# Kernel optimization log

Measured on AMD Instinct MI355X. Metric: run time of the kernel, lower is better.

Reference implementation:

```python
import jax, jax.numpy as jnp
import numpy as np

# --- physics constants (match init_kwargs) ---
LX = LY = 0.2
NX = NY = 256
DT = 2.5e-5
N_STEPS = 300
RHO = 1000.0
CS = 5.0
MU = RHO * CS * CS
ETA = 0.1
BULK_DAMPING = 0.01
SOURCE_SIGMA = 0.003
N_PML = 20
MAX_DAMPING = 0.05
PHYSICS_EPS = 1e-8
DX = LX / NX
DY = LY / NY
INV_DX = 1.0 / DX
INV_DY = 1.0 / DY
DT_OVER_RHO = DT / RHO


def _build_damping():
    # cosine-tapered PML profile, exactly as the torch loop
    i = jnp.arange(N_PML, dtype=jnp.float32)
    arg = jnp.pi * (N_PML - i) / N_PML
    factor = 1.0 - MAX_DAMPING * (0.5 + 0.5 * jnp.cos(arg))
    dx_prof = jnp.ones(NX, dtype=jnp.float32)
    dx_prof = dx_prof.at[:N_PML].set(factor)
    dx_prof = dx_prof.at[NX - N_PML:].set(factor[::-1])
    dy_prof = jnp.ones(NY, dtype=jnp.float32)
    dy_prof = dy_prof.at[:N_PML].set(factor)
    dy_prof = dy_prof.at[NY - N_PML:].set(factor[::-1])
    return jnp.outer(dx_prof, dy_prof)  # [nx, ny]


def _grids():
    x = jnp.linspace(DX / 2, LX - DX / 2, NX, dtype=jnp.float32)
    y = jnp.linspace(DY / 2, LY - DY / 2, NY, dtype=jnp.float32)
    return x[:, None], y[None, :]  # broadcastable grid_x, grid_y


def setup_inputs() -> dict:
    key = jax.random.key(0)
    # source trajectory in meters, kept inside the interior (away from PML)
    trajectory = 0.05 + 0.1 * jax.random.uniform(key, (N_STEPS, 2), dtype=jnp.float32)
    return {"trajectory": trajectory}


def reference(trajectory):
    damping = _build_damping()
    gx, gy = _grids()
    amp = 1.0

    def step(carry, xy):
        vz, strain_xz, strain_yz = carry  # each [nx, ny]
        x_t, y_t = xy[0], xy[1]
        # Gaussian source centered at (x_t, y_t)
        r_sq = (gx - x_t) ** 2 + (gy - y_t) ** 2
        source = amp * jnp.exp(-r_sq / (2.0 * SOURCE_SIGMA ** 2))
        # forward differences of vz (zero at trailing edge)
        dvz_dx = jnp.pad((vz[1:, :] - vz[:-1, :]) * INV_DX, ((0, 1), (0, 0)))
        dvz_dy = jnp.pad((vz[:, 1:] - vz[:, :-1]) * INV_DY, ((0, 0), (0, 1)))
        # Kelvin-Voigt stress
        strain_xz = strain_xz + dvz_dx * DT
        strain_yz = strain_yz + dvz_dy * DT
        sigma_xz = MU * strain_xz + ETA * dvz_dx
        sigma_yz = MU * strain_yz + ETA * dvz_dy
        # backward differences of stress (zero at leading edge)
        ds_dx = jnp.pad((sigma_xz[1:, :] - sigma_xz[:-1, :]) * INV_DX, ((1, 0), (0, 0)))
        ds_dy = jnp.pad((sigma_yz[:, 1:] - sigma_yz[:, :-1]) * INV_DY, ((0, 0), (1, 0)))
        # velocity update + bulk damping + PML damping
        vz = vz + DT_OVER_RHO * (ds_dx + ds_dy + source)
        vz = vz * (1.0 - BULK_DAMPING * DT)
        vz = vz * damping
        stress_mag = jnp.sqrt(sigma_xz ** 2 + sigma_yz ** 2 + PHYSICS_EPS)
        return (vz, strain_xz, strain_yz), (vz, stress_mag)

    z = jnp.zeros((NX, NY), dtype=jnp.float32)
    _, (vz_history, stress_history) = jax.lax.scan(step, (z, z, z), trajectory)
    return vz_history, stress_history
```

## Files before the change

kernel.cpp:

```cpp
#include <hip/hip_runtime.h>
#include <math.h>

typedef float v2f __attribute__((ext_vector_type(2)));

#define NX 256
#define NY 256
#define N_STEPS 300
#define N_CELLS (NX * NY)
#define TILE 16
#define HALO 8
#define LSTR 36
#define LROWS 34
#define LIDX(rr, cc) (((rr) + 1) * LSTR + ((cc) + 2))
#define NBX 16
#define NBY 16
#define NCHUNK 38

#define kINV_DX       1280.0f
#define kINV_DY       1280.0f
#define kDT           2.5e-5f
#define kMU           25000.0f
#define kETA          0.1f
#define kDT_OVER_RHO  2.5e-8f
#define kONE_MINUS_BD 0.99999975f
#define kNEG_INV_2SIG2 (-55555.5546875f)
#define kDX           7.8125e-4f
#define kEPS          1e-8f
#define kSRC_SKIP_D2  9.0e-4f

__device__ __forceinline__ float dprof(int k) {
    int m = min(k, NX - 1 - k);
    if (m >= 20) return 1.0f;
    float arg = 3.14159265358979f * (float)(20 - m) / 20.0f;
    return 1.0f - 0.05f * (0.5f + 0.5f * cosf(arg));
}

__device__ __forceinline__ void st_f2(float* p, v2f v) {
    union { v2f f; unsigned long long u; } x;
    x.f = v;
    __hip_atomic_store((unsigned long long*)p, x.u,
                       __ATOMIC_RELAXED, __HIP_MEMORY_SCOPE_AGENT);
}
__device__ __forceinline__ v2f ld_f2(const float* p) {
    union { unsigned long long u; v2f f; } x;
    x.u = __hip_atomic_load((const unsigned long long*)p,
                            __ATOMIC_RELAXED, __HIP_MEMORY_SCOPE_AGENT);
    return x.f;
}
__device__ __forceinline__ float ld_f1(const float* p) {
    union { unsigned u; float f; } x;
    x.u = __hip_atomic_load((const unsigned*)p,
                            __ATOMIC_RELAXED, __HIP_MEMORY_SCOPE_AGENT);
    return x.f;
}

__global__ __launch_bounds__(512, 1) void persist_kernel(
    const float2* __restrict__ traj,
    float* __restrict__ out,
    float* __restrict__ ws,
    unsigned* __restrict__ seq)
{
    __shared__ float s_vz[2][LROWS * LSTR];

    float* vzS[2]  = { ws + 0 * N_CELLS, ws + 1 * N_CELLS };
    float* sxzS[2] = { ws + 2 * N_CELLS, ws + 3 * N_CELLS };
    float* syzS[2] = { ws + 4 * N_CELLS, ws + 5 * N_CELLS };

    const int tid = threadIdx.x;
    const int bid = blockIdx.x;
    const int bx  = bid & (NBX - 1), by = bid >> 4;
    const int r   = tid >> 4;
    const int c0  = (tid & 15) << 1;

    const int gi  = by * TILE + r  - HALO;
    const int gj0 = bx * TILE + c0 - HALO;
    const int g   = gi * NY + gj0;

    const bool rowOK  = (gi >= 0) && (gi < NX);
    const bool colOK  = (gj0 >= 0) && (gj0 < NY);
    const bool inD    = rowOK && colOK;
    const bool haloUp   = (gi - 1 >= 0) && (gi - 1 < NX) && colOK;
    const bool haloLeft = rowOK && (gj0 - 1 >= 0);

    const float mxF  = (gi < NX - 1)      ? kINV_DX : 0.0f;
    const float myF1 = (gj0 + 1 < NY - 1) ? kINV_DY : 0.0f;
    const float mbX  = (gi > 0)           ? kINV_DX : 0.0f;
    const float mbY0 = (gj0 > 0)          ? kINV_DY : 0.0f;
    const v2f mx2  = {mxF, mxF};
    const v2f my2  = {kINV_DY, myF1};
    const v2f mbx2 = {mbX, mbX};
    const v2f mby2 = {mbY0, kINV_DY};

    const float dpx = rowOK ? dprof(gi) : 0.0f;
    const v2f damp2 = { inD ? dpx * dprof(gj0) * kONE_MINUS_BD : 0.0f,
                        inD ? dpx * dprof(gj0 + 1) * kONE_MINUS_BD : 0.0f };
    const float xi  = ((float)gi + 0.5f) * kDX;
    const v2f   yy2 = { ((float)gj0 + 0.5f) * kDX, ((float)gj0 + 1.5f) * kDX };

    const bool owned = (r >= HALO) && (r < HALO + TILE) &&
                       (c0 >= HALO) && (c0 + 1 < HALO + TILE);

    const float xlo = ((float)(by * TILE - HALO) + 0.5f) * kDX;
    const float xhi = ((float)(by * TILE + TILE + HALO - 1) + 0.5f) * kDX;
    const float ylo = ((float)(bx * TILE - HALO) + 0.5f) * kDX;
    const float yhi = ((float)(bx * TILE + TILE + HALO - 1) + 0.5f) * kDX;

    bool isPoller = false; int pollIdx = 0;
    if (tid < 8) {
        const int q  = tid + (tid >= 4);
        const int dy = q / 3 - 1, dx = q % 3 - 1;
        const int nbx_ = bx + dx, nby_ = by + dy;
        if (nbx_ >= 0 && nbx_ < NBX && nby_ >= 0 && nby_ < NBY) {
            isPoller = true;
            pollIdx = (nby_ * NBX + nbx_) * 4;
        }
    }

    for (int idx = tid; idx < 2 * LROWS * LSTR; idx += 512)
        ((float*)s_vz)[idx] = 0.0f;

    v2f V = {0.f, 0.f}, SX = {0.f, 0.f}, SY = {0.f, 0.f}, SXM = {0.f, 0.f};
    float symv = 0.f;
    __syncthreads();

    for (int ch = 0; ch < NCHUNK; ++ch) {
        if (ch > 0) {
            if (isPoller) {
                const unsigned tgt = (unsigned)ch;
                while (__hip_atomic_load(&seq[pollIdx], __ATOMIC_RELAXED,
                                         __HIP_MEMORY_SCOPE_AGENT) < tgt) {
                    __builtin_amdgcn_s_sleep(1);
                }
            }
            __syncthreads();

            if (!owned) {
                const int rs = (ch - 1) & 1;
                v2f nV = {0.f, 0.f}, nSX = {0.f, 0.f}, nSY = {0.f, 0.f};
                v2f nSXM = {0.f, 0.f};
                float nsym = 0.f;
                if (inD) {
                    nV  = ld_f2(&vzS[rs][g]);
                    nSX = ld_f2(&sxzS[rs][g]);
                    nSY = ld_f2(&syzS[rs][g]);
                }
                if (haloUp)   nSXM = ld_f2(&sxzS[rs][g - NY]);
                if (haloLeft) nsym = ld_f1(&syzS[rs][g - 1]);
                V = nV; SX = nSX; SY = nSY; SXM = nSXM; symv = nsym;
            }
        }

        *(v2f*)&s_vz[0][LIDX(r, c0)] = V;
        __syncthreads();

        const int t0 = ch * 8;
        float trx[8], tryy[8];
        #pragma unroll
        for (int s = 0; s < 8; ++s) {
            const int t = t0 + s;
            float2 t2 = (t < N_STEPS) ? traj[t] : make_float2(0.f, 0.f);
            trx[s] = t2.x; tryy[s] = t2.y;
        }

        bool srcNear = false;
        #pragma unroll
        for (int s = 0; s < 8; ++s) {
            const float ddx = fmaxf(fmaxf(xlo - trx[s], trx[s] - xhi), 0.0f);
            const float ddy = fmaxf(fmaxf(ylo - tryy[s], tryy[s] - yhi), 0.0f);
            if (ddx * ddx + ddy * ddy < kSRC_SKIP_D2) srcNear = true;
        }

        v2f hv[8], hs[8];
        #pragma unroll
        for (int s = 0; s < 8; ++s) {
            const int cur = s & 1, nxt = cur ^ 1;

            const v2f vp = *(const v2f*)&s_vz[cur][LIDX(r + 1, c0)];
            const v2f vm = *(const v2f*)&s_vz[cur][LIDX(r - 1, c0)];
            const float vr2 = s_vz[cur][LIDX(r, c0 + 2)];
            const float vl1 = s_vz[cur][LIDX(r, c0 - 1)];

            const v2f dvx = (vp - V) * mx2;
            const v2f vsh = {V.y, vr2};
            const v2f dvy = (vsh - V) * my2;

            SX += dvx * kDT;
            SY += dvy * kDT;
            const v2f GX = SX * kMU + dvx * kETA;
            const v2f GY = SY * kMU + dvy * kETA;

            const v2f dxm = (V - vm) * kINV_DX;
            SXM += dxm * kDT;
            const v2f GXM = SXM * kMU + dxm * kETA;
            const float dym = (V.x - vl1) * kINV_DY;
            symv += dym * kDT;
            const float gym = kMU * symv + kETA * dym;

            const v2f gsh = {gym, GX.x * 0.0f + GY.x};
            v2f ds = (GX - GXM) * mbx2 + (GY - gsh) * mby2;

            if (srcNear) {
                const float rx  = xi - trx[s];
                const float rx2 = rx * rx;
                const v2f ry  = yy2 - tryy[s];
                const v2f arg = (ry * ry + rx2) * kNEG_INV_2SIG2;
                ds += (v2f){__expf(arg.x), __expf(arg.y)};
            }

            V = (V + ds * kDT_OVER_RHO) * damp2;

            if (s < 7) *(v2f*)&s_vz[nxt][LIDX(r, c0)] = V;

            hv[s] = V;
            const v2f g2 = GX * GX + GY * GY + kEPS;
            hs[s] = (v2f){__builtin_amdgcn_sqrtf(g2.x),
                          __builtin_amdgcn_sqrtf(g2.y)};

            if (s < 7) __syncthreads();
        }

        if (owned && ch < NCHUNK - 1) {
            const int wsI = ch & 1;
            st_f2(&vzS[wsI][g],  V);
            st_f2(&sxzS[wsI][g], SX);
            st_f2(&syzS[wsI][g], SY);
        }
        __syncthreads();
        if (ch < NCHUNK - 1 && tid == 0) {
            __hip_atomic_store(&seq[bid * 4], (unsigned)(ch + 1),
                               __ATOMIC_RELAXED, __HIP_MEMORY_SCOPE_AGENT);
        }

        if (owned) {
            #pragma unroll
            for (int s = 0; s < 8; ++s) {
                if (t0 + s < N_STEPS) {
                    *(v2f*)&out[(size_t)(t0 + s) * N_CELLS + g] = hv[s];
                    *(v2f*)&out[(size_t)(N_STEPS + t0 + s) * N_CELLS + g] = hs[s];
                }
            }
        }
    }
}

extern "C" void kernel_launch(void* const* d_in, const int* in_sizes, int n_in,
                              void* d_out, int out_size, void* d_ws, size_t ws_size,
                              hipStream_t stream) {
    const float2* traj = (const float2*)d_in[0];
    float* out = (float*)d_out;
    float* ws  = (float*)d_ws;
    unsigned* seq = (unsigned*)((char*)d_ws + (size_t)6 * N_CELLS * sizeof(float));

    hipMemsetAsync(seq, 0, NBX * NBY * 4 * sizeof(unsigned), stream);

    void* args[] = { (void*)&traj, (void*)&out, (void*)&ws, (void*)&seq };
    hipLaunchCooperativeKernel((const void*)persist_kernel,
                               dim3(NBX * NBY), dim3(512), args, 0, stream);
}
```

Baseline: 194.0 us.

## Split tiles to 8x16 per block and use non-cooperative launch

Halves the owned tile height so the grid grows to 512 blocks of 384 threads, with launch bounds allowing up to three blocks per CU. This spreads the persistent stencil across more workgroups. The cooperative launch is replaced by a normal launch. It also drops a redundant multiply-by-zero term. The cost is more redundant halo computation per owned cell. The spin-wait sync between neighbouring blocks now assumes all blocks are co-resident without a cooperative-launch guarantee.

```diff
diff --git a/kernel.cpp b/kernel.cpp
--- a/kernel.cpp
+++ b/kernel.cpp
@@ -7,13 +7,17 @@
 #define NY 256
 #define N_STEPS 300
 #define N_CELLS (NX * NY)
-#define TILE 16
+#define TILE_R 8
+#define TILE_C 16
 #define HALO 8
+#define RROWS 24
 #define LSTR 36
-#define LROWS 34
+#define LROWS 26
 #define LIDX(rr, cc) (((rr) + 1) * LSTR + ((cc) + 2))
 #define NBX 16
-#define NBY 16
+#define NBY 32
+#define NBLKS (NBX * NBY)
+#define NTHREADS 384
 #define NCHUNK 38
 
 #define kINV_DX       1280.0f
@@ -54,7 +58,7 @@
     return x.f;
 }
 
-__global__ __launch_bounds__(512, 1) void persist_kernel(
+__global__ __launch_bounds__(NTHREADS, 3) void persist_kernel(
     const float2* __restrict__ traj,
     float* __restrict__ out,
     float* __restrict__ ws,
@@ -72,8 +76,8 @@
     const int r   = tid >> 4;
     const int c0  = (tid & 15) << 1;
 
-    const int gi  = by * TILE + r  - HALO;
-    const int gj0 = bx * TILE + c0 - HALO;
+    const int gi  = by * TILE_R + r  - HALO;
+    const int gj0 = bx * TILE_C + c0 - HALO;
     const int g   = gi * NY + gj0;
 
     const bool rowOK  = (gi >= 0) && (gi < NX);
@@ -97,13 +101,13 @@
     const float xi  = ((float)gi + 0.5f) * kDX;
     const v2f   yy2 = { ((float)gj0 + 0.5f) * kDX, ((float)gj0 + 1.5f) * kDX };
 
-    const bool owned = (r >= HALO) && (r < HALO + TILE) &&
-                       (c0 >= HALO) && (c0 + 1 < HALO + TILE);
-
-    const float xlo = ((float)(by * TILE - HALO) + 0.5f) * kDX;
-    const float xhi = ((float)(by * TILE + TILE + HALO - 1) + 0.5f) * kDX;
-    const float ylo = ((float)(bx * TILE - HALO) + 0.5f) * kDX;
-    const float yhi = ((float)(bx * TILE + TILE + HALO - 1) + 0.5f) * kDX;
+    const bool owned = (r >= HALO) && (r < HALO + TILE_R) &&
+                       (c0 >= HALO) && (c0 + 1 < HALO + TILE_C);
+
+    const float xlo = ((float)(by * TILE_R - HALO) + 0.5f) * kDX;
+    const float xhi = ((float)(by * TILE_R + TILE_R + HALO - 1) + 0.5f) * kDX;
+    const float ylo = ((float)(bx * TILE_C - HALO) + 0.5f) * kDX;
+    const float yhi = ((float)(bx * TILE_C + TILE_C + HALO - 1) + 0.5f) * kDX;
 
     bool isPoller = false; int pollIdx = 0;
     if (tid < 8) {
@@ -116,7 +120,7 @@
         }
     }
 
-    for (int idx = tid; idx < 2 * LROWS * LSTR; idx += 512)
+    for (int idx = tid; idx < 2 * LROWS * LSTR; idx += NTHREADS)
         ((float*)s_vz)[idx] = 0.0f;
 
     v2f V = {0.f, 0.f}, SX = {0.f, 0.f}, SY = {0.f, 0.f}, SXM = {0.f, 0.f};
@@ -196,7 +200,7 @@
             symv += dym * kDT;
             const float gym = kMU * symv + kETA * dym;
 
-            const v2f gsh = {gym, GX.x * 0.0f + GY.x};
+            const v2f gsh = {gym, GY.x};
             v2f ds = (GX - GXM) * mbx2 + (GY - gsh) * mby2;
 
             if (srcNear) {
@@ -251,9 +255,7 @@
     float* ws  = (float*)d_ws;
     unsigned* seq = (unsigned*)((char*)d_ws + (size_t)6 * N_CELLS * sizeof(float));
 
-    hipMemsetAsync(seq, 0, NBX * NBY * 4 * sizeof(unsigned), stream);
-
-    void* args[] = { (void*)&traj, (void*)&out, (void*)&ws, (void*)&seq };
-    hipLaunchCooperativeKernel((const void*)persist_kernel,
-                               dim3(NBX * NBY), dim3(512), args, 0, stream);
-}
+    hipMemsetAsync(seq, 0, NBLKS * 4 * sizeof(unsigned), stream);
+
+    persist_kernel<<<dim3(NBLKS), dim3(NTHREADS), 0, stream>>>(traj, out, ws, seq);
+}
```

After: 217.3 us. 12.0% more time.
